# Kernel tuning notes

Hardware: AMD Instinct MI355X
Metric: run time of the kernel (lower is better)

Reference implementation:

```python
import jax, jax.numpy as jnp
import numpy as np

SAMPLE_RATE = 0.1
BINS = int(256 * SAMPLE_RATE)  # 25
KSIZE = 7
EPS = 1e-6


def _pascal_kernel_2d(ksize):
    # kornia get_pascal_kernel_2d(ksize, norm=True): outer product of binomial row, sum=1
    row = np.array([1.0, 6.0, 15.0, 20.0, 15.0, 6.0, 1.0], dtype=np.float32)
    row = row / row.sum()
    k2d = np.outer(row, row)
    return jnp.asarray(k2d, dtype=jnp.float32)


def _blur_pool2d(x, ksize=KSIZE):
    # kornia.filters.blur_pool2d: depthwise conv with pascal kernel, stride 2, zero pad ksize//2
    C = x.shape[1]
    k = jnp.broadcast_to(_pascal_kernel_2d(ksize).astype(x.dtype), (C, 1, ksize, ksize))
    pad = ksize // 2
    return jax.lax.conv_general_dilated(
        x, k, window_strides=(2, 2), padding=((pad, pad), (pad, pad)),
        feature_group_count=C, dimension_numbers=("NCHW", "OIHW", "NCHW"))


def _per_channel_hist(x, bins):
    # torch.histc(v, bins, 0, 1) per (b, c) plane: values outside [0,1] ignored,
    # value == 1 falls in last bin. Fused via one flat scatter-add.
    B, C, H, W = x.shape
    v = x.reshape(B * C, H * W)
    idx = jnp.clip(jnp.floor(v * bins).astype(jnp.int32), 0, bins - 1)
    valid = ((v >= 0.0) & (v <= 1.0)).astype(x.dtype)
    flat_idx = (jnp.arange(B * C, dtype=jnp.int32)[:, None] * bins + idx).reshape(-1)
    hist = jnp.zeros(B * C * bins, dtype=x.dtype).at[flat_idx].add(valid.reshape(-1))
    return hist.reshape(B, C, bins)


def setup_inputs() -> dict:
    key = jax.random.key(0)
    kx, ky = jax.random.split(key)
    B, C, H, W = 32, 3, 512, 512
    x = jax.random.uniform(kx, (B, C, H, W), dtype=jnp.float32)
    y = jax.random.uniform(ky, (B, C, H, W), dtype=jnp.float32)
    return {"x": x, "y": y}


def reference(x, y):
    hw = x.shape[-2] * x.shape[-1]  # original H*W (as in source)
    xb = _blur_pool2d(x)
    yb = _blur_pool2d(y)
    xh = _per_channel_hist(xb, BINS) / hw  # [B, C, BINS]
    yh = _per_channel_hist(yb, BINS) / hw
    # nn.CosineSimilarity(dim=0, eps=1e-6) applied per (b, c) vector pair
    dot = jnp.sum(xh * yh, axis=-1)
    nx = jnp.maximum(jnp.linalg.norm(xh, axis=-1), EPS)
    ny = jnp.maximum(jnp.linalg.norm(yh, axis=-1), EPS)
    cos = dot / (nx * ny)  # [B, C]
    return jnp.mean(cos)
```

## Files before the change

### kernel.cpp

```cpp
#include <hip/hip_runtime.h>

#define BINS 25
#define H 512
#define W 512
#define NPLANES 96
#define NSH 32
#define BPP 8

__global__ __launch_bounds__(256) void blur_hist(
        const float* __restrict__ x, const float* __restrict__ y,
        unsigned int* __restrict__ partial) {
    const int b = blockIdx.x;
    const int z = b >> 3;
    const float* src = (z < NPLANES) ? x + (size_t)z * H * W
                                     : y + (size_t)(z - NPLANES) * H * W;

    __shared__ unsigned int sh[NSH * BINS];
    const int tid = threadIdx.x;
    if (tid < (NSH * BINS / 4))
        *(float4*)((float*)sh + 4 * tid) = make_float4(0.f, 0.f, 0.f, 0.f);
    __syncthreads();

    const int i = tid & 63;
    const int s = (b & 7) * 4 + (tid >> 6);
    const int c0 = 8 * i - 4;
    const int o0 = (i == 0)  ? 0   : c0;
    const int o3 = (i == 63) ? 508 : c0 + 12;
    const float m0 = (i == 0)  ? 0.f : 1.f;
    const float m3 = (i == 63) ? 0.f : 1.f;

    const float w0 = 1.f/64.f, w1 = 6.f/64.f, w2 = 15.f/64.f, w3 = 20.f/64.f;

    auto load_row = [&](int gy) -> float4 {
        float4 h = make_float4(0.f, 0.f, 0.f, 0.f);
        if ((unsigned)gy < (unsigned)H) {
            const float* rp = src + (size_t)gy * W;
            float4 Q0 = *(const float4*)(rp + o0);
            float4 Q1 = *(const float4*)(rp + c0 + 4);
            float4 Q2 = *(const float4*)(rp + c0 + 8);
            float4 Q3 = *(const float4*)(rp + o3);
            float r1 = Q0.y * m0, r2 = Q0.z * m0, r3 = Q0.w * m0;
            float r4 = Q1.x, r5 = Q1.y, r6 = Q1.z, r7 = Q1.w;
            float r8 = Q2.x, r9 = Q2.y, r10 = Q2.z, r11 = Q2.w;
            float r12 = Q3.x * m3, r13 = Q3.y * m3;
            h.x = w0*(r1 + r7)  + w1*(r2 + r6)  + w2*(r3 + r5)  + w3*r4;
            h.y = w0*(r3 + r9)  + w1*(r4 + r8)  + w2*(r5 + r7)  + w3*r6;
            h.z = w0*(r5 + r11) + w1*(r6 + r10) + w2*(r7 + r9)  + w3*r8;
            h.w = w0*(r7 + r13) + w1*(r8 + r12) + w2*(r9 + r11) + w3*r10;
        }
        return h;
    };

    unsigned int* wh = sh + (tid & (NSH - 1)) * BINS;
    auto binit = [&](float v) {
        int bb = min((int)(v * 25.f), BINS - 1);
        atomicAdd(&wh[bb], 1u);
    };
    auto vout = [&](const float4& h0, const float4& h1, const float4& h2,
                    const float4& h3, const float4& h4, const float4& h5,
                    const float4& h6) {
        binit(w0*(h0.x+h6.x) + w1*(h1.x+h5.x) + w2*(h2.x+h4.x) + w3*h3.x);
        binit(w0*(h0.y+h6.y) + w1*(h1.y+h5.y) + w2*(h2.y+h4.y) + w3*h3.y);
        binit(w0*(h0.z+h6.z) + w1*(h1.z+h5.z) + w2*(h2.z+h4.z) + w3*h3.z);
        binit(w0*(h0.w+h6.w) + w1*(h1.w+h5.w) + w2*(h2.w+h4.w) + w3*h3.w);
    };

    const int gy0 = 16 * s - 3;
    float4 h0 = load_row(gy0 + 0), h1 = load_row(gy0 + 1), h2 = load_row(gy0 + 2),
           h3 = load_row(gy0 + 3), h4 = load_row(gy0 + 4), h5 = load_row(gy0 + 5),
           h6 = load_row(gy0 + 6);
    #pragma unroll
    for (int j = 0; j < 7; j++) {
        float4 hA = load_row(gy0 + 7 + 2 * j);
        float4 hB = load_row(gy0 + 8 + 2 * j);
        vout(h0, h1, h2, h3, h4, h5, h6);
        h0 = h2; h1 = h3; h2 = h4; h3 = h5; h4 = h6; h5 = hA; h6 = hB;
    }
    vout(h0, h1, h2, h3, h4, h5, h6);
    __syncthreads();

    if (tid < BINS) {
        unsigned int acc = 0;
        #pragma unroll
        for (int g = 0; g < NSH; g++) acc += sh[g * BINS + tid];
        partial[b * BINS + tid] = acc;
    }
}

__global__ __launch_bounds__(64) void reduce_cos(
        const unsigned int* __restrict__ partial, float* __restrict__ out) {
    __shared__ float sa[BINS], sb[BINS];
    const int p = blockIdx.x;
    const int t = threadIdx.x;
    if (t < BINS) {
        unsigned int a = 0, bb = 0;
        #pragma unroll
        for (int j = 0; j < BPP; j++) {
            a  += partial[((size_t)p * BPP + j) * BINS + t];
            bb += partial[((size_t)(NPLANES + p) * BPP + j) * BINS + t];
        }
        sa[t] = (float)a;
        sb[t] = (float)bb;
    }
    __syncthreads();
    if (t == 0) {
        const float inv_hw = 1.0f / (float)(H * W);
        float dot = 0.f, nx = 0.f, ny = 0.f;
        for (int k = 0; k < BINS; k++) {
            float a = sa[k] * inv_hw;
            float c = sb[k] * inv_hw;
            dot += a * c;
            nx  += a * a;
            ny  += c * c;
        }
        nx = fmaxf(sqrtf(nx), 1e-6f);
        ny = fmaxf(sqrtf(ny), 1e-6f);
        atomicAdd(out, (dot / (nx * ny)) * (1.0f / (float)NPLANES));
    }
}

extern "C" void kernel_launch(void* const* d_in, const int* in_sizes, int n_in,
                              void* d_out, int out_size, void* d_ws, size_t ws_size,
                              hipStream_t stream) {
    const float* x = (const float*)d_in[0];
    const float* y = (const float*)d_in[1];
    float* out = (float*)d_out;

    unsigned int* partial = (unsigned int*)d_ws;

    hipMemsetAsync(out, 0, sizeof(float), stream);

    blur_hist<<<2 * NPLANES * BPP, 256, 0, stream>>>(x, y, partial);
    reduce_cos<<<NPLANES, 64, 0, stream>>>(partial, out);
}
```

Baseline: 220.1 us.

## Stage input rows through LDS ring with async global_load_lds pipelining

Replaces direct per-thread global float4 loads with asynchronous global-to-LDS loads into a per-wave 6-row ring buffer. A swizzled layout avoids bank conflicts, and manual waitcnt tokens overlap the next row fetches with compute. Each wave now processes 16 output rows instead of 8, with 4 blocks per plane and an interleaved block order. This aims to hide memory latency and remove the redundant overlapping loads. It relies on fragile inline waitcnt counting and uses more LDS per block, which may lower occupancy.

```diff
diff --git a/kernel.cpp b/kernel.cpp
--- a/kernel.cpp
+++ b/kernel.cpp
@@ -5,49 +5,75 @@
 #define W 512
 #define NPLANES 96
 #define NSH 32
-#define BPP 8
+#define BPP 4
+#define RING 6
+
+typedef const __attribute__((address_space(1))) void* gvp;
+typedef __attribute__((address_space(3))) void* lvp;
 
 __global__ __launch_bounds__(256) void blur_hist(
         const float* __restrict__ x, const float* __restrict__ y,
         unsigned int* __restrict__ partial) {
-    const int b = blockIdx.x;
-    const int z = b >> 3;
+    const int b = ((blockIdx.x & 7) * 96) + (blockIdx.x >> 3);
+    const int z = b >> 2;
     const float* src = (z < NPLANES) ? x + (size_t)z * H * W
                                      : y + (size_t)(z - NPLANES) * H * W;
 
+    __shared__ __align__(16) float ring[4][RING][512];
     __shared__ unsigned int sh[NSH * BINS];
+
     const int tid = threadIdx.x;
     if (tid < (NSH * BINS / 4))
         *(float4*)((float*)sh + 4 * tid) = make_float4(0.f, 0.f, 0.f, 0.f);
     __syncthreads();
 
-    const int i = tid & 63;
-    const int s = (b & 7) * 4 + (tid >> 6);
-    const int c0 = 8 * i - 4;
-    const int o0 = (i == 0)  ? 0   : c0;
-    const int o3 = (i == 63) ? 508 : c0 + 12;
-    const float m0 = (i == 0)  ? 0.f : 1.f;
-    const float m3 = (i == 63) ? 0.f : 1.f;
+    const int l  = tid & 63;
+    const int wv = tid >> 6;
+    const int S  = (b & 3) * 4 + wv;
+    const int g0 = 32 * S - 3;
+
+    auto swz = [](int c) { return c ^ ((c >> 3) & 7) ^ (((c >> 6) & 1) << 2); };
+
+    const int so0 = swz(l) * 4;
+    const int so1 = swz(64 + l) * 4;
+
+    float* const rbase = &ring[wv][0][0];
+
+    auto STAGE = [&](int k, int sl) {
+        int gy = g0 + k;
+        gy = min(max(gy, 0), H - 1);
+        const float* rp = src + (size_t)gy * W;
+        float* lp = rbase + sl * 512;
+        __builtin_amdgcn_global_load_lds((gvp)(rp + so0), (lvp)lp,         16, 0, 0);
+        __builtin_amdgcn_global_load_lds((gvp)(rp + so1), (lvp)(lp + 256), 16, 0, 0);
+    };
+
+    const int p0 = swz(max(2 * l - 1, 0));
+    const int p1 = swz(2 * l);
+    const int p2 = swz(2 * l + 1);
+    const int p3 = swz(min(2 * l + 2, 127));
+    const float m0 = (l == 0)  ? 0.f : 1.f;
+    const float m3 = (l == 63) ? 0.f : 1.f;
 
     const float w0 = 1.f/64.f, w1 = 6.f/64.f, w2 = 15.f/64.f, w3 = 20.f/64.f;
 
-    auto load_row = [&](int gy) -> float4 {
-        float4 h = make_float4(0.f, 0.f, 0.f, 0.f);
-        if ((unsigned)gy < (unsigned)H) {
-            const float* rp = src + (size_t)gy * W;
-            float4 Q0 = *(const float4*)(rp + o0);
-            float4 Q1 = *(const float4*)(rp + c0 + 4);
-            float4 Q2 = *(const float4*)(rp + c0 + 8);
-            float4 Q3 = *(const float4*)(rp + o3);
-            float r1 = Q0.y * m0, r2 = Q0.z * m0, r3 = Q0.w * m0;
-            float r4 = Q1.x, r5 = Q1.y, r6 = Q1.z, r7 = Q1.w;
-            float r8 = Q2.x, r9 = Q2.y, r10 = Q2.z, r11 = Q2.w;
-            float r12 = Q3.x * m3, r13 = Q3.y * m3;
-            h.x = w0*(r1 + r7)  + w1*(r2 + r6)  + w2*(r3 + r5)  + w3*r4;
-            h.y = w0*(r3 + r9)  + w1*(r4 + r8)  + w2*(r5 + r7)  + w3*r6;
-            h.z = w0*(r5 + r11) + w1*(r6 + r10) + w2*(r7 + r9)  + w3*r8;
-            h.w = w0*(r7 + r13) + w1*(r8 + r12) + w2*(r9 + r11) + w3*r10;
-        }
+    auto HROW = [&](int k, int sl) -> float4 {
+        const float* rp = rbase + sl * 512;
+        const float4 qa = *(const float4*)(rp + 4 * p0);
+        const float4 qb = *(const float4*)(rp + 4 * p1);
+        const float4 qc = *(const float4*)(rp + 4 * p2);
+        const float4 qd = *(const float4*)(rp + 4 * p3);
+        const int gy = g0 + k;
+        const float rm = ((unsigned)gy < (unsigned)H) ? 1.f : 0.f;
+        float r1 = qa.y * m0, r2 = qa.z * m0, r3 = qa.w * m0;
+        float r4 = qb.x, r5 = qb.y, r6 = qb.z, r7 = qb.w;
+        float r8 = qc.x, r9 = qc.y, r10 = qc.z, r11 = qc.w;
+        float r12 = qd.x * m3, r13 = qd.y * m3;
+        float4 h;
+        h.x = (w0*(r1 + r7)  + w1*(r2 + r6)  + w2*(r3 + r5)  + w3*r4)  * rm;
+        h.y = (w0*(r3 + r9)  + w1*(r4 + r8)  + w2*(r5 + r7)  + w3*r6)  * rm;
+        h.z = (w0*(r5 + r11) + w1*(r6 + r10) + w2*(r7 + r9)  + w3*r8)  * rm;
+        h.w = (w0*(r7 + r13) + w1*(r8 + r12) + w2*(r9 + r11) + w3*r10) * rm;
         return h;
     };
 
@@ -65,18 +91,28 @@
         binit(w0*(h0.w+h6.w) + w1*(h1.w+h5.w) + w2*(h2.w+h4.w) + w3*h3.w);
     };
 
-    const int gy0 = 16 * s - 3;
-    float4 h0 = load_row(gy0 + 0), h1 = load_row(gy0 + 1), h2 = load_row(gy0 + 2),
-           h3 = load_row(gy0 + 3), h4 = load_row(gy0 + 4), h5 = load_row(gy0 + 5),
-           h6 = load_row(gy0 + 6);
+    STAGE(0, 0); STAGE(1, 1); STAGE(2, 2);
+    STAGE(3, 3); STAGE(4, 4); STAGE(5, 5);
+    asm volatile("s_waitcnt vmcnt(2)" ::: "memory");
+    float4 h0 = HROW(0, 0), h1 = HROW(1, 1), h2 = HROW(2, 2),
+           h3 = HROW(3, 3), h4 = HROW(4, 4);
+    asm volatile("s_waitcnt lgkmcnt(0)" ::: "memory");
+    STAGE(6, 0); STAGE(7, 1); STAGE(8, 2); STAGE(9, 3);
+
+    float4 h5, h6;
     #pragma unroll
-    for (int j = 0; j < 7; j++) {
-        float4 hA = load_row(gy0 + 7 + 2 * j);
-        float4 hB = load_row(gy0 + 8 + 2 * j);
+    for (int j = 0; j < 16; j++) {
+        const int k5 = 2 * j + 5, k6 = 2 * j + 6;
+        asm volatile("s_waitcnt vmcnt(6)" ::: "memory");
+        h5 = HROW(k5, k5 % RING);
+        h6 = HROW(k6, k6 % RING);
+        asm volatile("s_waitcnt lgkmcnt(0)" ::: "memory");
+        STAGE(2 * j + 10, (2 * j + 10) % RING);
+        STAGE(2 * j + 11, (2 * j + 11) % RING);
         vout(h0, h1, h2, h3, h4, h5, h6);
-        h0 = h2; h1 = h3; h2 = h4; h3 = h5; h4 = h6; h5 = hA; h6 = hB;
+        h0 = h2; h1 = h3; h2 = h4; h3 = h5; h4 = h6;
     }
-    vout(h0, h1, h2, h3, h4, h5, h6);
+    asm volatile("s_waitcnt vmcnt(0)" ::: "memory");
     __syncthreads();
 
     if (tid < BINS) {
```

Result: no change. 220.7 us (+0.3%).
